# Optimization experiments

Measured on AMD Instinct MI355X. Metric: run time of the kernel, lower is better.

Reference implementation:

```python
import jax, jax.numpy as jnp
import numpy as np
from jax import lax

K = 3
STRIDE = 1
PAD = 1
DIL = 1


def _rrsvm(x, s):
    # x: [B, C, H, W], s: [C, K, K]
    B, C, H, W = x.shape
    # im2col: [B, C*K*K, Ho, Wo], channel-major patch ordering -> reshape (C, K*K)
    patches = lax.conv_general_dilated_patches(
        x, (K, K), (STRIDE, STRIDE), [(PAD, PAD), (PAD, PAD)],
        rhs_dilation=(DIL, DIL))
    Ho, Wo = patches.shape[2], patches.shape[3]
    p = patches.reshape(B, C, K * K, Ho, Wo)
    # descending sort of each window's values (rank pooling order)
    order = jnp.argsort(-p, axis=2)                      # [B, C, K*K, Ho, Wo]
    sorted_p = jnp.take_along_axis(p, order, axis=2)
    # learned per-rank weights, per channel
    out = jnp.einsum('bckhw,ck->bchw', sorted_p, s.reshape(C, K * K))
    indices = jnp.transpose(order, (0, 1, 3, 4, 2))      # [B, C, Ho, Wo, K*K]
    return out, indices


def setup_inputs() -> dict:
    key = jax.random.key(0)
    k1, k2 = jax.random.split(key)
    B, C, H, W = 16, 128, 56, 56
    x = jax.random.normal(k1, (B, C, H, W), dtype=jnp.float32)
    # module inits s to 1/(C*K*K); use random positive weights for a non-degenerate test
    s = jax.random.uniform(k2, (C, K, K), dtype=jnp.float32) / (K * K)
    return {"x": x, "s": s}


def reference(x, s):
    return _rrsvm(x, s)
```

## Files before the change

kernel.cpp:

```cpp
#include <hip/hip_runtime.h>


#define B_ 16
#define C_ 128
#define H_ 56
#define W_ 56
#define NPIX (B_*C_*H_*W_)
#define BLK 256
#define PXT 4

typedef float v4f __attribute__((ext_vector_type(4)));

__device__ __forceinline__ void sort9(float v[9], float id[9]) {
    #pragma unroll
    for (int rnd = 0; rnd < 9; ++rnd) {
        #pragma unroll
        for (int i = (rnd & 1); i + 1 < 9; i += 2) {
            float vi = v[i], vj = v[i + 1];
            float ii = id[i], ij = id[i + 1];
            bool sw = vj > vi;
            v[i]      = sw ? vj : vi;  v[i + 1]  = sw ? vi : vj;
            id[i]     = sw ? ij : ii;  id[i + 1] = sw ? ii : ij;
        }
    }
}

__global__ __launch_bounds__(BLK) void rrsvm_kernel(
    const float* __restrict__ x, const float* __restrict__ s,
    float* __restrict__ out, float* __restrict__ idxout)
{
    const int gtid = blockIdx.x * BLK + threadIdx.x;
    const int pix0 = gtid * PXT;
    const int w0   = pix0 % W_;
    const int t    = pix0 / W_;
    const int h    = t % H_;
    const int bc   = t / H_;
    const int c    = bc & (C_ - 1);

    const float* sp = s + c * 9;
    float sw9[9];
    #pragma unroll
    for (int r = 0; r < 9; ++r) sw9[r] = sp[r];

    const float* img = x + (size_t)bc * (H_ * W_);
    const int r0 = (h > 0)      ? h - 1 : 0;
    const int r2 = (h < H_ - 1) ? h + 1 : H_ - 1;
    const int cl = (w0 > 0)        ? w0 - 1 : 0;
    const int cr = (w0 < W_ - PXT) ? w0 + 4 : W_ - 1;
    const float* p0 = img + r0 * W_;
    const float* p1 = img + h  * W_;
    const float* p2 = img + r2 * W_;

    float T[3][6];
    {
        v4f m0 = *(const v4f*)(p0 + w0);
        v4f m1 = *(const v4f*)(p1 + w0);
        v4f m2 = *(const v4f*)(p2 + w0);
        T[0][0] = p0[cl]; T[0][1] = m0.x; T[0][2] = m0.y; T[0][3] = m0.z; T[0][4] = m0.w; T[0][5] = p0[cr];
        T[1][0] = p1[cl]; T[1][1] = m1.x; T[1][2] = m1.y; T[1][3] = m1.z; T[1][4] = m1.w; T[1][5] = p1[cr];
        T[2][0] = p2[cl]; T[2][1] = m2.x; T[2][2] = m2.y; T[2][3] = m2.z; T[2][4] = m2.w; T[2][5] = p2[cr];
    }

    const bool rv0 = (h > 0), rv2 = (h < H_ - 1);
    const bool cvL = (w0 > 0), cvR = (w0 < W_ - PXT);
    #pragma unroll
    for (int j = 0; j < 6; ++j) {
        T[0][j] = rv0 ? T[0][j] : 0.0f;
        T[2][j] = rv2 ? T[2][j] : 0.0f;
    }
    T[0][0] = cvL ? T[0][0] : 0.0f;
    T[1][0] = cvL ? T[1][0] : 0.0f;
    T[2][0] = cvL ? T[2][0] : 0.0f;
    T[0][5] = cvR ? T[0][5] : 0.0f;
    T[1][5] = cvR ? T[1][5] : 0.0f;
    T[2][5] = cvR ? T[2][5] : 0.0f;

    float idxf[36];
    v4f o;
    float oacc[4];

    #pragma unroll
    for (int j = 0; j < PXT; ++j) {
        float v[9]  = { T[0][j], T[0][j+1], T[0][j+2],
                        T[1][j], T[1][j+1], T[1][j+2],
                        T[2][j], T[2][j+1], T[2][j+2] };
        float id[9] = { 0, 1, 2, 3, 4, 5, 6, 7, 8 };
        sort9(v, id);
        float acc = 0.0f;
        #pragma unroll
        for (int r = 0; r < 9; ++r) acc = fmaf(v[r], sw9[r], acc);
        oacc[j] = acc;
        #pragma unroll
        for (int r = 0; r < 9; ++r) idxf[j * 9 + r] = id[r];
    }
    o.x = oacc[0]; o.y = oacc[1]; o.z = oacc[2]; o.w = oacc[3];

    *(v4f*)(out + pix0) = o;

    v4f* dst = (v4f*)(idxout + (size_t)gtid * 36);
    const v4f* srcv = (const v4f*)idxf;
    #pragma unroll
    for (int k = 0; k < 9; ++k)
        dst[k] = srcv[k];
}

extern "C" void kernel_launch(void* const* d_in, const int* in_sizes, int n_in,
                              void* d_out, int out_size, void* d_ws, size_t ws_size,
                              hipStream_t stream) {
    const float* x = (const float*)d_in[0];
    const float* s = (const float*)d_in[1];
    float* out    = (float*)d_out;
    float* idxout = out + NPIX;

    const int nblocks = NPIX / (BLK * PXT);
    rrsvm_kernel<<<nblocks, BLK, 0, stream>>>(x, s, out, idxout);
}
```

Measured before the change: 325.2 us.

## Stage index output through LDS for coalesced nontemporal stores

Each thread now writes its 36 sort indices into shared memory, and after a barrier the block writes the whole tile to global memory with consecutive threads storing consecutive 16-byte vectors. The old code had each thread write a 144-byte strided run, so the writes were poorly coalesced. The output and index writes also become nontemporal stores so they bypass the caches. The cost is 36 KB of LDS per block, which limits occupancy, plus an added barrier.

```diff
diff --git a/kernel.cpp b/kernel.cpp
--- a/kernel.cpp
+++ b/kernel.cpp
@@ -8,6 +8,7 @@
 #define NPIX (B_*C_*H_*W_)
 #define BLK 256
 #define PXT 4
+#define PXB (BLK * PXT)
 
 typedef float v4f __attribute__((ext_vector_type(4)));
 
@@ -29,7 +30,10 @@
     const float* __restrict__ x, const float* __restrict__ s,
     float* __restrict__ out, float* __restrict__ idxout)
 {
-    const int gtid = blockIdx.x * BLK + threadIdx.x;
+    __shared__ float lds[PXB * 9];
+
+    const int tid  = threadIdx.x;
+    const int gtid = blockIdx.x * BLK + tid;
     const int pix0 = gtid * PXT;
     const int w0   = pix0 % W_;
     const int t    = pix0 / W_;
@@ -75,10 +79,8 @@
     T[1][5] = cvR ? T[1][5] : 0.0f;
     T[2][5] = cvR ? T[2][5] : 0.0f;
 
-    float idxf[36];
-    v4f o;
+    v4f q[9];
     float oacc[4];
-
     #pragma unroll
     for (int j = 0; j < PXT; ++j) {
         float v[9]  = { T[0][j], T[0][j+1], T[0][j+2],
@@ -91,17 +93,27 @@
         for (int r = 0; r < 9; ++r) acc = fmaf(v[r], sw9[r], acc);
         oacc[j] = acc;
         #pragma unroll
-        for (int r = 0; r < 9; ++r) idxf[j * 9 + r] = id[r];
+        for (int r = 0; r < 9; ++r) {
+            const int f = j * 9 + r;
+            q[f >> 2][f & 3] = id[r];
+        }
     }
-    o.x = oacc[0]; o.y = oacc[1]; o.z = oacc[2]; o.w = oacc[3];
+    v4f o; o.x = oacc[0]; o.y = oacc[1]; o.z = oacc[2]; o.w = oacc[3];
 
-    *(v4f*)(out + pix0) = o;
+    __builtin_nontemporal_store(o, (v4f*)(out + pix0));
 
-    v4f* dst = (v4f*)(idxout + (size_t)gtid * 36);
-    const v4f* srcv = (const v4f*)idxf;
+    v4f* lw = (v4f*)(lds + (size_t)tid * 36);
     #pragma unroll
     for (int k = 0; k < 9; ++k)
-        dst[k] = srcv[k];
+        lw[k] = q[k];
+
+    __syncthreads();
+
+    v4f* dst = (v4f*)(idxout + (size_t)blockIdx.x * (PXB * 9));
+    const v4f* src = (const v4f*)lds;
+    #pragma unroll
+    for (int k = 0; k < 9; ++k)
+        __builtin_nontemporal_store(src[tid + k * 256], dst + tid + k * 256);
 }
 
 extern "C" void kernel_launch(void* const* d_in, const int* in_sizes, int n_in,
@@ -112,6 +124,6 @@
     float* out    = (float*)d_out;
     float* idxout = out + NPIX;
 
-    const int nblocks = NPIX / (BLK * PXT);
+    const int nblocks = NPIX / PXB;
     rrsvm_kernel<<<nblocks, BLK, 0, stream>>>(x, s, out, idxout);
 }
```

After: 291.1 us. -10.5%, faster.
